# Optimization experiments

Hardware: AMD Instinct MI355X
Metric: run time of the kernel (lower is better)

Reference implementation:

```python
import jax, jax.numpy as jnp
import numpy as np

B, C_IN, C_OUT, E, H, W = 64, 384, 384, 8, 28, 28


def setup_inputs() -> dict:
    key = jax.random.key(0)
    k1, k2, k3 = jax.random.split(key, 3)
    x = jax.random.normal(k1, (B, C_IN, H, W), dtype=jnp.float32)
    routing_weights = jax.random.uniform(k2, (B, E), dtype=jnp.float32)
    # kaiming_normal_(mode='fan_out') per expert: std = sqrt(2 / fan_out), fan_out = out_channels * 1 * 1
    std = float(np.sqrt(2.0 / C_OUT))
    weight = jax.random.normal(k3, (E, C_OUT, C_IN), dtype=jnp.float32) * std
    return {"x": x, "routing_weights": routing_weights, "weight": weight}


def reference(x, routing_weights, weight):
    # Per-sample aggregated 1x1 conv weights: [b, c_out, c_in]
    agg = jnp.einsum('be,eoi->boi', routing_weights, weight)
    # Per-sample channel mixing (1x1 conv with groups=b == batched GEMM)
    out = jnp.einsum('boi,bihw->bohw', agg, x)
    return out
```

## Files before the change

kernel.cpp:

```cpp
#include <hip/hip_runtime.h>
#include <cstdint>

#define B_   64
#define CI_  384
#define CO_  384
#define HW_  784
#define E_   8

typedef unsigned short ushort_t;
typedef unsigned int   uint_t;

typedef __attribute__((ext_vector_type(8))) short bf16x8;
typedef __attribute__((ext_vector_type(4))) float f32x4;

__device__ __forceinline__ ushort_t f2bf_rne(float f) {
  uint_t u = __builtin_bit_cast(uint_t, f);
  u += 0x7fffu + ((u >> 16) & 1u);
  return (ushort_t)(u >> 16);
}

__device__ __forceinline__ uint_t pack_bf16_trunc(float f0, float f1) {
  return __builtin_amdgcn_perm(__builtin_bit_cast(uint_t, f1),
                               __builtin_bit_cast(uint_t, f0),
                               0x07060302u);
}

__global__ __launch_bounds__(256) void agg_kernel(const float* __restrict__ rw,
                                                  const float* __restrict__ w,
                                                  ushort_t* __restrict__ agg) {
  __shared__ float r[B_ * E_];
  const int tid = threadIdx.x;
  r[tid]       = rw[tid];
  r[tid + 256] = rw[tid + 256];
  const int base = blockIdx.x * 512 + tid * 2;
  float2 wv[E_];
#pragma unroll
  for (int e = 0; e < E_; ++e)
    wv[e] = *(const float2*)&w[e * (CO_ * CI_) + base];
  __syncthreads();
#pragma unroll 4
  for (int b = 0; b < B_; ++b) {
    float ax = 0.f, ay = 0.f;
#pragma unroll
    for (int e = 0; e < E_; ++e) {
      const float rv = r[b * E_ + e];
      ax += rv * wv[e].x;
      ay += rv * wv[e].y;
    }
    const uint_t v = (uint_t)f2bf_rne(ax) | ((uint_t)f2bf_rne(ay) << 16);
    *(uint_t*)&agg[(size_t)b * (CO_ * CI_) + base] = v;
  }
}

#define BM 128
#define BN 128
#define BK 32
#define KIT (CI_ / BK)
#define BS_STRIDE 40

__global__ __launch_bounds__(256) void moe_gemm(const float* __restrict__ X,
                                                const ushort_t* __restrict__ Agg,
                                                float* __restrict__ Out) {
  __shared__ __align__(16) ushort_t As[BM * BK];
  __shared__ __align__(16) ushort_t Bs[BN * BS_STRIDE];

  const int tid  = threadIdx.x;
  const int lane = tid & 63;
  const int wave = tid >> 6;
  const int wm = wave & 1, wn = wave >> 1;
  const int b = blockIdx.z, mt = blockIdx.y, nt = blockIdx.x;

  const ushort_t* Ab = Agg + (size_t)b * CO_ * CI_ + mt * BM * CI_;
  const float*    Xb = X   + (size_t)b * CI_ * HW_;

  const int sn  = tid & 127;
  const int sk4 = (tid >> 7) * 4;
  const int gn  = nt * BN + sn;
  const int gnc = gn < HW_ ? gn : (HW_ - 1);
  const float* Xcol = Xb + gnc;

  f32x4 acc[4][4];
#pragma unroll
  for (int i = 0; i < 4; ++i)
#pragma unroll
    for (int j = 0; j < 4; ++j)
      acc[i][j] = (f32x4)0.f;

  const int l15 = lane & 15;
  const int lq  = lane >> 4;

  for (int kk = 0; kk < KIT; ++kk) {
    const int k0 = kk * BK;
#pragma unroll
    for (int j = 0; j < 2; ++j) {
      const int idx = tid + j * 256;
      const int m = idx >> 2, q = idx & 3;
      const ushort_t* src = Ab + m * CI_ + k0 + q * 8;
      __builtin_amdgcn_global_load_lds(
          (const __attribute__((address_space(1))) uint_t*)src,
          (__attribute__((address_space(3))) uint_t*)&As[idx * 8], 16, 0, 0);
    }
#pragma unroll
    for (int j = 0; j < 4; ++j) {
      const int kl = j * 8 + sk4;
      const float* p = Xcol + (size_t)(k0 + kl) * HW_;
      const float v0 = p[0], v1 = p[HW_], v2 = p[2 * HW_], v3 = p[3 * HW_];
      const uint_t lo = pack_bf16_trunc(v0, v1);
      const uint_t hi = pack_bf16_trunc(v2, v3);
      *(uint2*)&Bs[sn * BS_STRIDE + kl] = make_uint2(lo, hi);
    }
    __syncthreads();
    bf16x8 a[4], bb[4];
#pragma unroll
    for (int mf = 0; mf < 4; ++mf)
      a[mf] = *(const bf16x8*)&As[(wm * 64 + mf * 16 + l15) * BK + lq * 8];
#pragma unroll
    for (int nf = 0; nf < 4; ++nf)
      bb[nf] = *(const bf16x8*)&Bs[(wn * 64 + nf * 16 + l15) * BS_STRIDE + lq * 8];
#pragma unroll
    for (int mf = 0; mf < 4; ++mf)
#pragma unroll
      for (int nf = 0; nf < 4; ++nf)
        acc[mf][nf] = __builtin_amdgcn_mfma_f32_16x16x32_bf16(a[mf], bb[nf],
                                                              acc[mf][nf], 0, 0, 0);
    __syncthreads();
  }

  float* Ob = Out + (size_t)b * CO_ * HW_;
#pragma unroll
  for (int mf = 0; mf < 4; ++mf) {
#pragma unroll
    for (int nf = 0; nf < 4; ++nf) {
      const int n = nt * BN + wn * 64 + nf * 16 + l15;
      if (n < HW_) {
        const int mbase = mt * BM + wm * 64 + mf * 16 + lq * 4;
#pragma unroll
        for (int r = 0; r < 4; ++r)
          Ob[(size_t)(mbase + r) * HW_ + n] = acc[mf][nf][r];
      }
    }
  }
}

extern "C" void kernel_launch(void* const* d_in, const int* in_sizes, int n_in,
                              void* d_out, int out_size, void* d_ws, size_t ws_size,
                              hipStream_t stream) {
  const float* x  = (const float*)d_in[0];
  const float* rw = (const float*)d_in[1];
  const float* w  = (const float*)d_in[2];
  float* out = (float*)d_out;
  ushort_t* agg = (ushort_t*)d_ws;

  agg_kernel<<<dim3((CO_ * CI_) / 512), 256, 0, stream>>>(rw, w, agg);
  moe_gemm<<<dim3(7, 3, B_), 256, 0, stream>>>(x, agg, out);
}
```

Measured before the change: 190.6 us.

## Swizzle A-tile LDS layout, remap GEMM grid, split agg kernel over batch

Stores the bf16 A tile in LDS with an XOR swizzle on the 16-byte chunk index, so the MFMA fragment reads hit fewer LDS bank conflicts. The GEMM grid is remapped so that 8 consecutive batches share the same m/n tile position in launch order, which is meant to improve cache locality and spread work across XCDs. The aggregation kernel is split across 4 batch groups, giving 4x more blocks for parallelism at the cost of reloading the expert weights in each group.

```diff
diff --git a/kernel.cpp b/kernel.cpp
--- a/kernel.cpp
+++ b/kernel.cpp
@@ -38,8 +38,10 @@
   for (int e = 0; e < E_; ++e)
     wv[e] = *(const float2*)&w[e * (CO_ * CI_) + base];
   __syncthreads();
+  const int b0 = blockIdx.y * 16;
 #pragma unroll 4
-  for (int b = 0; b < B_; ++b) {
+  for (int bi = 0; bi < 16; ++bi) {
+    const int b = b0 + bi;
     float ax = 0.f, ay = 0.f;
 #pragma unroll
     for (int e = 0; e < E_; ++e) {
@@ -68,7 +70,14 @@
   const int lane = tid & 63;
   const int wave = tid >> 6;
   const int wm = wave & 1, wn = wave >> 1;
-  const int b = blockIdx.z, mt = blockIdx.y, nt = blockIdx.x;
+
+  const int bx = blockIdx.x;
+  const int by = blockIdx.y;
+  const int bg  = by / 21;
+  const int rem = by - bg * 21;
+  const int mt  = rem / 7;
+  const int nt  = rem - mt * 7;
+  const int b   = bg * 8 + bx;
 
   const ushort_t* Ab = Agg + (size_t)b * CO_ * CI_ + mt * BM * CI_;
   const float*    Xb = X   + (size_t)b * CI_ * HW_;
@@ -88,17 +97,22 @@
 
   const int l15 = lane & 15;
   const int lq  = lane >> 4;
+  const int xqA = lq ^ ((l15 >> 1) & 3);
+
+  const int sm0 = tid >> 2,           sq0 = (tid & 3) ^ ((tid >> 3) & 3);
+  const int sm1 = (tid + 256) >> 2,   sq1 = (tid & 3) ^ (((tid + 256) >> 3) & 3);
 
   for (int kk = 0; kk < KIT; ++kk) {
     const int k0 = kk * BK;
-#pragma unroll
-    for (int j = 0; j < 2; ++j) {
-      const int idx = tid + j * 256;
-      const int m = idx >> 2, q = idx & 3;
-      const ushort_t* src = Ab + m * CI_ + k0 + q * 8;
+    {
+      const ushort_t* src0 = Ab + sm0 * CI_ + k0 + sq0 * 8;
       __builtin_amdgcn_global_load_lds(
-          (const __attribute__((address_space(1))) uint_t*)src,
-          (__attribute__((address_space(3))) uint_t*)&As[idx * 8], 16, 0, 0);
+          (const __attribute__((address_space(1))) uint_t*)src0,
+          (__attribute__((address_space(3))) uint_t*)&As[tid * 8], 16, 0, 0);
+      const ushort_t* src1 = Ab + sm1 * CI_ + k0 + sq1 * 8;
+      __builtin_amdgcn_global_load_lds(
+          (const __attribute__((address_space(1))) uint_t*)src1,
+          (__attribute__((address_space(3))) uint_t*)&As[(tid + 256) * 8], 16, 0, 0);
     }
 #pragma unroll
     for (int j = 0; j < 4; ++j) {
@@ -112,8 +126,10 @@
     __syncthreads();
     bf16x8 a[4], bb[4];
 #pragma unroll
-    for (int mf = 0; mf < 4; ++mf)
-      a[mf] = *(const bf16x8*)&As[(wm * 64 + mf * 16 + l15) * BK + lq * 8];
+    for (int mf = 0; mf < 4; ++mf) {
+      const int m = wm * 64 + mf * 16 + l15;
+      a[mf] = *(const bf16x8*)&As[(m * 4 + xqA) * 8];
+    }
 #pragma unroll
     for (int nf = 0; nf < 4; ++nf)
       bb[nf] = *(const bf16x8*)&Bs[(wn * 64 + nf * 16 + l15) * BS_STRIDE + lq * 8];
@@ -151,6 +167,6 @@
   float* out = (float*)d_out;
   ushort_t* agg = (ushort_t*)d_ws;
 
-  agg_kernel<<<dim3((CO_ * CI_) / 512), 256, 0, stream>>>(rw, w, agg);
-  moe_gemm<<<dim3(7, 3, B_), 256, 0, stream>>>(x, agg, out);
+  agg_kernel<<<dim3((CO_ * CI_) / 512, 4), 256, 0, stream>>>(rw, w, agg);
+  moe_gemm<<<dim3(8, 168), 256, 0, stream>>>(x, agg, out);
 }
```

New measurement: 175.9 us. 1.08x faster.
